# Kernel optimization log

Hardware: AMD Instinct MI355X
Metric: run time of the kernel (lower is better)

## Reference

```python
import jax, jax.numpy as jnp
import numpy as np

N = 50000
E = 1600000
F_IN = 4
F_OUT = 32
PERIODS = 12


def setup_inputs() -> dict:
    key = jax.random.key(0)
    ks = jax.random.split(key, 18)
    s_in = 1.0 / np.sqrt(F_IN)
    s_cat = 1.0 / np.sqrt(2 * F_OUT)
    s_out = 1.0 / np.sqrt(F_OUT)
    inp = {
        'x': jax.random.normal(ks[0], (N, F_IN, PERIODS), dtype=jnp.float32),
        'edge_index': jax.random.randint(ks[1], (2, E), 0, N, dtype=jnp.int32),
        'attention': jax.random.uniform(ks[2], (PERIODS,), dtype=jnp.float32),
        # GRU update gate z: GCNConv weight/bias + Linear(2*F_OUT -> F_OUT)
        'Wz': jax.random.normal(ks[3], (F_IN, F_OUT), jnp.float32) * s_in,
        'bz': jnp.zeros((F_OUT,), jnp.float32),
        'Lz': jax.random.normal(ks[4], (2 * F_OUT, F_OUT), jnp.float32) * s_cat,
        'lz': jnp.zeros((F_OUT,), jnp.float32),
        # reset gate r
        'Wr': jax.random.normal(ks[5], (F_IN, F_OUT), jnp.float32) * s_in,
        'br': jnp.zeros((F_OUT,), jnp.float32),
        'Lr': jax.random.normal(ks[6], (2 * F_OUT, F_OUT), jnp.float32) * s_cat,
        'lr': jnp.zeros((F_OUT,), jnp.float32),
        # candidate h
        'Wh': jax.random.normal(ks[7], (F_IN, F_OUT), jnp.float32) * s_in,
        'bh': jnp.zeros((F_OUT,), jnp.float32),
        'Lh': jax.random.normal(ks[8], (2 * F_OUT, F_OUT), jnp.float32) * s_cat,
        'lh': jnp.zeros((F_OUT,), jnp.float32),
        # outer Linear(32 -> periods)
        'Wo': jax.random.normal(ks[9], (F_OUT, PERIODS), jnp.float32) * s_out,
        'bo': jnp.zeros((PERIODS,), jnp.float32),
    }
    return inp


def reference(x, edge_index, attention, Wz, bz, Lz, lz, Wr, br, Lr, lr, Wh, bh, Lh, lh, Wo, bo):
    n = x.shape[0]
    # gcn_norm: add self loops, symmetric D^-1/2 (A+I) D^-1/2
    loop = jnp.arange(n, dtype=edge_index.dtype)
    row = jnp.concatenate([edge_index[0], loop])  # source
    col = jnp.concatenate([edge_index[1], loop])  # target
    w = jnp.ones(row.shape[0], dtype=x.dtype)
    deg = jax.ops.segment_sum(w, col, num_segments=n)
    dinv = jnp.where(deg > 0, jax.lax.rsqrt(deg), 0.0)
    norm = dinv[row] * dinv[col]  # [E+N]

    def conv(xt, W, b):
        h = xt @ W                                   # [N, F_OUT]
        msg = h[row] * norm[:, None]                 # gather + scale
        return jax.ops.segment_sum(msg, col, num_segments=n) + b

    H0 = jnp.zeros((n, F_OUT), dtype=x.dtype)  # A3TGCN passes H=None each period

    def tgcn(xt):
        Z = jax.nn.sigmoid(jnp.concatenate([conv(xt, Wz, bz), H0], axis=1) @ Lz + lz)
        R = jax.nn.sigmoid(jnp.concatenate([conv(xt, Wr, br), H0], axis=1) @ Lr + lr)
        Ht = jnp.tanh(jnp.concatenate([conv(xt, Wh, bh), H0 * R], axis=1) @ Lh + lh)
        return Z * H0 + (1.0 - Z) * Ht

    Hs = jax.vmap(tgcn)(jnp.moveaxis(x, 2, 0))       # [T, N, F_OUT]
    probs = jax.nn.softmax(attention)
    H = jnp.einsum('tnc,t->nc', Hs, probs)           # attention-weighted sum over periods
    return jax.nn.relu(H) @ Wo + bo                  # [N, PERIODS]
```

## Files before the change

kernel.cpp:

```cpp
#include <hip/hip_runtime.h>
#include <hip/hip_fp16.h>
#include <math.h>

#define CHUNK 6144
#define CAPG  10240
#define GNODES 21

union U2H { uint2 u; __half2 h[2]; };

__global__ void k_pre(const float* __restrict__ Wz, const float* __restrict__ Lz, const float* __restrict__ lz,
                      const float* __restrict__ Wh, const float* __restrict__ Lh, const float* __restrict__ lh,
                      const float* __restrict__ bz, const float* __restrict__ bh,
                      const float* __restrict__ att,
                      float* __restrict__ AzT, float* __restrict__ AhT,
                      float* __restrict__ bzp, float* __restrict__ bhp, float* __restrict__ probs,
                      int* __restrict__ gcur) {
  int t = threadIdx.x;
  gcur[t] = 0;
  if (t < 128) {
    int f = t >> 2, k = t & 3;
    float s = 0.f, s2 = 0.f;
    for (int j = 0; j < 32; ++j) {
      s  = fmaf(Wz[k * 32 + j], Lz[j * 32 + f], s);
      s2 = fmaf(Wh[k * 32 + j], Lh[j * 32 + f], s2);
    }
    AzT[t] = s; AhT[t] = s2;
  }
  if (t >= 128 && t < 160) {
    int f = t - 128;
    float s = lz[f], s2 = lh[f];
    for (int j = 0; j < 32; ++j) {
      s  = fmaf(bz[j], Lz[j * 32 + f], s);
      s2 = fmaf(bh[j], Lh[j * 32 + f], s2);
    }
    bzp[f] = s; bhp[f] = s2;
  }
  if (t == 160) {
    float m = att[0];
    for (int i = 1; i < 12; ++i) m = fmaxf(m, att[i]);
    float e[12]; float s = 0.f;
    for (int i = 0; i < 12; ++i) { e[i] = __expf(att[i] - m); s += e[i]; }
    for (int i = 0; i < 12; ++i) probs[i] = e[i] / s;
  }
}

__global__ __launch_bounds__(1024) void k_part(const int* __restrict__ row, const int* __restrict__ col,
                                               int E, int nbkt,
                                               int* __restrict__ gcur, unsigned* __restrict__ part) {
  __shared__ unsigned spak[CHUNK];
  __shared__ unsigned char sbkt[CHUNK];
  __shared__ unsigned char slc[CHUNK];
  __shared__ int hist[256], sscan[256], scur[256], gbase[256];
  int t = threadIdx.x;
  int base = blockIdx.x * CHUNK;
  int cnt = E - base; if (cnt > CHUNK) cnt = CHUNK;
  if (t < 256) hist[t] = 0;
  __syncthreads();
  for (int i = t; i < cnt; i += 1024) {
    int c = col[base + i];
    int b = c >> 8;
    sbkt[i] = (unsigned char)b;
    slc[i]  = (unsigned char)(c & 255);
    atomicAdd(&hist[b], 1);
  }
  __syncthreads();
  int v = 0;
  if (t < 256) { v = hist[t]; sscan[t] = v; }
  __syncthreads();
  for (int off = 1; off < 256; off <<= 1) {
    int a = 0;
    if (t < 256 && t >= off) a = sscan[t - off];
    __syncthreads();
    if (t < 256) sscan[t] += a;
    __syncthreads();
  }
  if (t < 256) {
    sscan[t] -= v;
    gbase[t] = (v > 0) ? atomicAdd(&gcur[t], v) : 0;
    scur[t] = 0;
  }
  __syncthreads();
  for (int i = t; i < cnt; i += 1024) {
    int r = row[base + i];
    int b = sbkt[i];
    int pos = atomicAdd(&scur[b], 1);
    spak[sscan[b] + pos] = ((unsigned)r << 8) | (unsigned)slc[i];
  }
  __syncthreads();
  int wave = t >> 6, lane = t & 63;
  for (int b = wave; b < nbkt; b += 16) {
    int len = hist[b], gb = gbase[b], src = sscan[b];
    int lim = CAPG - gb; if (lim > len) lim = len;
    unsigned* dst = part + (size_t)b * CAPG + gb;
    for (int j = lane; j < lim; j += 64) dst[j] = spak[src + j];
  }
}

__global__ __launch_bounds__(1024) void k_sort(const unsigned* __restrict__ part, const int* __restrict__ gcur,
                                               const float4* __restrict__ x4,
                                               int* __restrict__ csr, int2* __restrict__ rng,
                                               float* __restrict__ dinv, uint2* __restrict__ xh2, int n) {
  __shared__ unsigned sedge[CAPG];
  __shared__ int hist[256], soff[256], scur2[256];
  __shared__ float sdi[256];
  int b = blockIdx.x, t = threadIdx.x;
  int cnt = gcur[b]; if (cnt > CAPG) cnt = CAPG;
  const unsigned* src = part + (size_t)b * CAPG;
  if (t < 256) hist[t] = 0;
  __syncthreads();
  for (int i = t; i < cnt; i += 1024) {
    unsigned e = src[i];
    sedge[i] = e;
    atomicAdd(&hist[e & 255u], 1);
  }
  __syncthreads();
  int v = 0;
  if (t < 256) { v = hist[t]; soff[t] = v; }
  __syncthreads();
  for (int off = 1; off < 256; off <<= 1) {
    int a = 0;
    if (t < 256 && t >= off) a = soff[t - off];
    __syncthreads();
    if (t < 256) soff[t] += a;
    __syncthreads();
  }
  int base = b * CAPG;
  if (t < 256) {
    int excl = soff[t] - v;
    int node = b * 256 + t;
    float di = rsqrtf((float)(v + 1));
    sdi[t] = di;
    if (node < n) {
      rng[node] = make_int2(base + excl, base + excl + v);
      dinv[node] = di;
    }
    soff[t] = excl;
    scur2[t] = 0;
  }
  __syncthreads();
  for (int i = t; i < cnt; i += 1024) {
    unsigned e = sedge[i];
    int lc = (int)(e & 255u);
    int pos = atomicAdd(&scur2[lc], 1);
    csr[base + soff[lc] + pos] = (int)(e >> 8);
  }
  int gb = b * 3072;
  for (int j = t; j < 3072; j += 1024) {
    int gi = gb + j;
    if (gi < n * 12) {
      float4 f = x4[gi];
      float d = sdi[j / 12];
      __half2 h0 = __floats2half2_rn(d * f.x, d * f.y);
      __half2 h1 = __floats2half2_rn(d * f.z, d * f.w);
      uint2 u; u.x = *(unsigned*)&h0; u.y = *(unsigned*)&h1;
      xh2[gi] = u;
    }
  }
}

__global__ __launch_bounds__(256) void k_gather(const int* __restrict__ csr, const int2* __restrict__ rng,
                                                const float* __restrict__ dinv, const uint2* __restrict__ xh2,
                                                const float* __restrict__ AzT, const float* __restrict__ AhT,
                                                const float* __restrict__ bzp, const float* __restrict__ bhp,
                                                const float* __restrict__ probs,
                                                const float* __restrict__ Wo, const float* __restrict__ bo,
                                                float* __restrict__ out, int n) {
  __shared__ float sY[GNODES * 49];
  __shared__ float sH[GNODES * 33];
  __shared__ float4 sAz4[32], sAh4[32];
  __shared__ float sbzp[32], sbhp[32], sprobs[12], sbo[12], sWo[384];
  int t = threadIdx.x;
  int nb = blockIdx.x * GNODES;

  if (t < 32) {
    sAz4[t] = ((const float4*)AzT)[t];
    sAh4[t] = ((const float4*)AhT)[t];
    sbzp[t] = bzp[t]; sbhp[t] = bhp[t];
  }
  if (t >= 32 && t < 44) { sprobs[t - 32] = probs[t - 32]; sbo[t - 32] = bo[t - 32]; }
  for (int i = t; i < 384; i += 256) sWo[i] = Wo[i];

  int grp = t / 12, c = t - grp * 12;
  int node = nb + grp;
  if (grp < GNODES && node < n) {
    U2H s; s.u = xh2[(size_t)node * 12 + c];
    float2 f0 = __half22float2(s.h[0]), f1 = __half22float2(s.h[1]);
    float a0 = f0.x, a1 = f0.y, a2 = f1.x, a3 = f1.y;
    int2 r = rng[node];
    int e = r.x, end = r.y;
#define ACC4(V) { \
    float2 g0 = __half22float2(V.h[0]), g1 = __half22float2(V.h[1]); \
    a0 += g0.x; a1 += g0.y; a2 += g1.x; a3 += g1.y; }
    for (; e + 8 <= end; e += 8) {
      int r0 = csr[e],     r1 = csr[e + 1], r2 = csr[e + 2], r3 = csr[e + 3];
      int r4 = csr[e + 4], r5 = csr[e + 5], r6 = csr[e + 6], r7 = csr[e + 7];
      U2H v0, v1, v2, v3, v4, v5, v6, v7;
      v0.u = xh2[(size_t)r0 * 12 + c];
      v1.u = xh2[(size_t)r1 * 12 + c];
      v2.u = xh2[(size_t)r2 * 12 + c];
      v3.u = xh2[(size_t)r3 * 12 + c];
      v4.u = xh2[(size_t)r4 * 12 + c];
      v5.u = xh2[(size_t)r5 * 12 + c];
      v6.u = xh2[(size_t)r6 * 12 + c];
      v7.u = xh2[(size_t)r7 * 12 + c];
      ACC4(v0) ACC4(v1) ACC4(v2) ACC4(v3) ACC4(v4) ACC4(v5) ACC4(v6) ACC4(v7)
    }
    for (; e < end; ++e) {
      int r0 = csr[e];
      U2H v0; v0.u = xh2[(size_t)r0 * 12 + c];
      ACC4(v0)
    }
#undef ACC4
    float di = dinv[node];
    float* yb = sY + grp * 49 + c * 4;
    yb[0] = a0 * di; yb[1] = a1 * di; yb[2] = a2 * di; yb[3] = a3 * di;
  }
  __syncthreads();

  for (int u = t; u < GNODES * 32; u += 256) {
    int ln = u >> 5, f = u & 31;
    if (nb + ln >= n) continue;
    const float* y = sY + ln * 49;
    float4 az = sAz4[f], ah = sAh4[f];
    float bzf = sbzp[f], bhf = sbhp[f];
    float acc = 0.f;
#pragma unroll
    for (int tt = 0; tt < 12; ++tt) {
      float y0 = y[tt], y1 = y[12 + tt], y2 = y[24 + tt], y3 = y[36 + tt];
      float za = fmaf(az.x, y0, fmaf(az.y, y1, fmaf(az.z, y2, fmaf(az.w, y3, bzf))));
      float ha = fmaf(ah.x, y0, fmaf(ah.y, y1, fmaf(ah.z, y2, fmaf(ah.w, y3, bhf))));
      float ez = __expf(za);
      float ax = fabsf(ha);
      float e2 = __expf(-2.f * ax);
      float g = (1.f - e2) / ((1.f + ez) * (1.f + e2));
      acc = fmaf(sprobs[tt], copysignf(g, ha), acc);
    }
    sH[ln * 33 + f] = fmaxf(acc, 0.f);
  }
  __syncthreads();

  if (t < GNODES * 12) {
    int ln = t / 12, p = t - ln * 12;
    int node2 = nb + ln;
    if (node2 < n) {
      float acc = sbo[p];
      const float* h = sH + ln * 33;
      const float* wv = sWo + p;
#pragma unroll
      for (int f2 = 0; f2 < 32; ++f2) acc = fmaf(h[f2], wv[f2 * 12], acc);
      out[node2 * 12 + p] = acc;
    }
  }
}

extern "C" void kernel_launch(void* const* d_in, const int* in_sizes, int n_in,
                              void* d_out, int out_size, void* d_ws, size_t ws_size,
                              hipStream_t stream) {
  const float* x   = (const float*)d_in[0];
  const int*   ei  = (const int*)d_in[1];
  const float* att = (const float*)d_in[2];
  const float* Wz  = (const float*)d_in[3];
  const float* bz  = (const float*)d_in[4];
  const float* Lz  = (const float*)d_in[5];
  const float* lz  = (const float*)d_in[6];
  const float* Wh  = (const float*)d_in[11];
  const float* bh  = (const float*)d_in[12];
  const float* Lh  = (const float*)d_in[13];
  const float* lh  = (const float*)d_in[14];
  const float* Wo  = (const float*)d_in[15];
  const float* bo  = (const float*)d_in[16];
  float* out = (float*)d_out;

  const int N = in_sizes[0] / (4 * 12);
  const int E = in_sizes[1] / 2;
  const int NBKT = (N + 255) >> 8;
  const int* row = ei;
  const int* col = ei + E;

  char* w = (char*)d_ws;
  size_t o = 0;
  auto alloc = [&](size_t bytes) -> char* {
    o = (o + 255) & ~(size_t)255;
    char* p = w + o; o += bytes; return p;
  };
  float* pAzT   = (float*)alloc(128 * 4);
  float* pAhT   = (float*)alloc(128 * 4);
  float* pbzp   = (float*)alloc(32 * 4);
  float* pbhp   = (float*)alloc(32 * 4);
  float* pprobs = (float*)alloc(12 * 4);
  int*   pgcur  = (int*)alloc(256 * 4);
  float* pdinv  = (float*)alloc((size_t)NBKT * 256 * 4);
  int2*  prng   = (int2*)alloc((size_t)N * 8);
  unsigned* ppart = (unsigned*)alloc((size_t)256 * CAPG * 4);
  int*   pcsr   = (int*)alloc((size_t)256 * CAPG * 4);
  uint2* pxh    = (uint2*)alloc((size_t)NBKT * 256 * 12 * 8);
  (void)ws_size; (void)n_in; (void)out_size;

  k_pre<<<1, 256, 0, stream>>>(Wz, Lz, lz, Wh, Lh, lh, bz, bh, att,
                               pAzT, pAhT, pbzp, pbhp, pprobs, pgcur);
  k_part<<<(E + CHUNK - 1) / CHUNK, 1024, 0, stream>>>(row, col, E, NBKT, pgcur, ppart);
  k_sort<<<NBKT, 1024, 0, stream>>>(ppart, pgcur, (const float4*)x, pcsr, prng, pdinv, pxh, N);
  k_gather<<<(N + GNODES - 1) / GNODES, 256, 0, stream>>>(pcsr, prng, pdinv, pxh,
                                                          pAzT, pAhT, pbzp, pbhp, pprobs,
                                                          Wo, bo, out, N);
}
```

Before: 170.0 us.

## Split CSR sort into degree scan and parallel atomic scatter kernels

Per-node in-degrees are now counted with global atomics during partitioning. A small kernel scans these degrees to produce row ranges, cursors, dinv and the scaled half-precision features. A separate scatter kernel then places edges into CSR slots using global atomic cursors, with several blocks per bucket. This replaces the single shared-memory counting sort per bucket, whose grid was smaller than the GPU, with a more parallel scatter. In exchange it adds about 3.2M global atomics, and neighbour order within a row becomes nondeterministic. CSR entries are also stored pre-multiplied by 12 so the gather kernel skips that index multiply.

```diff
diff --git a/kernel.cpp b/kernel.cpp
--- a/kernel.cpp
+++ b/kernel.cpp
@@ -4,6 +4,7 @@
 
 #define CHUNK 6144
 #define CAPG  10240
+#define SCATB 5
 #define GNODES 21
 
 union U2H { uint2 u; __half2 h[2]; };
@@ -46,7 +47,8 @@
 
 __global__ __launch_bounds__(1024) void k_part(const int* __restrict__ row, const int* __restrict__ col,
                                                int E, int nbkt,
-                                               int* __restrict__ gcur, unsigned* __restrict__ part) {
+                                               int* __restrict__ gcur, unsigned* __restrict__ part,
+                                               int* __restrict__ deg) {
   __shared__ unsigned spak[CHUNK];
   __shared__ unsigned char sbkt[CHUNK];
   __shared__ unsigned char slc[CHUNK];
@@ -62,6 +64,7 @@
     sbkt[i] = (unsigned char)b;
     slc[i]  = (unsigned char)(c & 255);
     atomicAdd(&hist[b], 1);
+    atomicAdd(&deg[c], 1);
   }
   __syncthreads();
   int v = 0;
@@ -96,65 +99,60 @@
   }
 }
 
-__global__ __launch_bounds__(1024) void k_sort(const unsigned* __restrict__ part, const int* __restrict__ gcur,
-                                               const float4* __restrict__ x4,
-                                               int* __restrict__ csr, int2* __restrict__ rng,
-                                               float* __restrict__ dinv, uint2* __restrict__ xh2, int n) {
-  __shared__ unsigned sedge[CAPG];
-  __shared__ int hist[256], soff[256], scur2[256];
+__global__ __launch_bounds__(256) void k_dinv(const int* __restrict__ deg, const float4* __restrict__ x4,
+                                              int2* __restrict__ rng, int* __restrict__ cursor,
+                                              float* __restrict__ dinv, uint2* __restrict__ xh2, int n) {
+  __shared__ int s[256];
   __shared__ float sdi[256];
   int b = blockIdx.x, t = threadIdx.x;
-  int cnt = gcur[b]; if (cnt > CAPG) cnt = CAPG;
-  const unsigned* src = part + (size_t)b * CAPG;
-  if (t < 256) hist[t] = 0;
-  __syncthreads();
-  for (int i = t; i < cnt; i += 1024) {
-    unsigned e = src[i];
-    sedge[i] = e;
-    atomicAdd(&hist[e & 255u], 1);
-  }
-  __syncthreads();
-  int v = 0;
-  if (t < 256) { v = hist[t]; soff[t] = v; }
+  int node = b * 256 + t;
+  int d = (node < n) ? deg[node] : 0;
+  s[t] = d;
   __syncthreads();
   for (int off = 1; off < 256; off <<= 1) {
-    int a = 0;
-    if (t < 256 && t >= off) a = soff[t - off];
+    int a = (t >= off) ? s[t - off] : 0;
     __syncthreads();
-    if (t < 256) soff[t] += a;
+    s[t] += a;
     __syncthreads();
   }
+  int excl = s[t] - d;
   int base = b * CAPG;
-  if (t < 256) {
-    int excl = soff[t] - v;
-    int node = b * 256 + t;
-    float di = rsqrtf((float)(v + 1));
-    sdi[t] = di;
-    if (node < n) {
-      rng[node] = make_int2(base + excl, base + excl + v);
-      dinv[node] = di;
-    }
-    soff[t] = excl;
-    scur2[t] = 0;
-  }
-  __syncthreads();
-  for (int i = t; i < cnt; i += 1024) {
-    unsigned e = sedge[i];
-    int lc = (int)(e & 255u);
-    int pos = atomicAdd(&scur2[lc], 1);
-    csr[base + soff[lc] + pos] = (int)(e >> 8);
-  }
+  float di = rsqrtf((float)(d + 1));
+  sdi[t] = di;
+  if (node < n) {
+    rng[node] = make_int2(base + excl, base + excl + d);
+    cursor[node] = base + excl;
+    dinv[node] = di;
+  }
+  __syncthreads();
   int gb = b * 3072;
-  for (int j = t; j < 3072; j += 1024) {
+  for (int j = t; j < 3072; j += 256) {
     int gi = gb + j;
     if (gi < n * 12) {
       float4 f = x4[gi];
-      float d = sdi[j / 12];
-      __half2 h0 = __floats2half2_rn(d * f.x, d * f.y);
-      __half2 h1 = __floats2half2_rn(d * f.z, d * f.w);
+      float dd = sdi[j / 12];
+      __half2 h0 = __floats2half2_rn(dd * f.x, dd * f.y);
+      __half2 h1 = __floats2half2_rn(dd * f.z, dd * f.w);
       uint2 u; u.x = *(unsigned*)&h0; u.y = *(unsigned*)&h1;
       xh2[gi] = u;
     }
+  }
+}
+
+__global__ __launch_bounds__(512) void k_scat(const unsigned* __restrict__ part, const int* __restrict__ gcur,
+                                              int* __restrict__ cursor, int* __restrict__ csr, int nbkt) {
+  int b = blockIdx.x % nbkt;
+  int j = blockIdx.x / nbkt;
+  int cnt = gcur[b]; if (cnt > CAPG) cnt = CAPG;
+  int i0 = j * 2048;
+  int i1 = i0 + 2048; if (i1 > cnt) i1 = cnt;
+  const unsigned* src = part + (size_t)b * CAPG;
+  int lim = (b + 1) * CAPG;
+  for (int i = i0 + threadIdx.x; i < i1; i += 512) {
+    unsigned e = src[i];
+    int node = b * 256 + (int)(e & 255u);
+    int pos = atomicAdd(&cursor[node], 1);
+    if (pos < lim) csr[pos] = (int)(e >> 8) * 12;
   }
 }
 
@@ -183,7 +181,8 @@
   int grp = t / 12, c = t - grp * 12;
   int node = nb + grp;
   if (grp < GNODES && node < n) {
-    U2H s; s.u = xh2[(size_t)node * 12 + c];
+    const uint2* xb = xh2 + c;
+    U2H s; s.u = xb[(size_t)node * 12];
     float2 f0 = __half22float2(s.h[0]), f1 = __half22float2(s.h[1]);
     float a0 = f0.x, a1 = f0.y, a2 = f1.x, a3 = f1.y;
     int2 r = rng[node];
@@ -195,19 +194,13 @@
       int r0 = csr[e],     r1 = csr[e + 1], r2 = csr[e + 2], r3 = csr[e + 3];
       int r4 = csr[e + 4], r5 = csr[e + 5], r6 = csr[e + 6], r7 = csr[e + 7];
       U2H v0, v1, v2, v3, v4, v5, v6, v7;
-      v0.u = xh2[(size_t)r0 * 12 + c];
-      v1.u = xh2[(size_t)r1 * 12 + c];
-      v2.u = xh2[(size_t)r2 * 12 + c];
-      v3.u = xh2[(size_t)r3 * 12 + c];
-      v4.u = xh2[(size_t)r4 * 12 + c];
-      v5.u = xh2[(size_t)r5 * 12 + c];
-      v6.u = xh2[(size_t)r6 * 12 + c];
-      v7.u = xh2[(size_t)r7 * 12 + c];
+      v0.u = xb[r0]; v1.u = xb[r1]; v2.u = xb[r2]; v3.u = xb[r3];
+      v4.u = xb[r4]; v5.u = xb[r5]; v6.u = xb[r6]; v7.u = xb[r7];
       ACC4(v0) ACC4(v1) ACC4(v2) ACC4(v3) ACC4(v4) ACC4(v5) ACC4(v6) ACC4(v7)
     }
     for (; e < end; ++e) {
       int r0 = csr[e];
-      U2H v0; v0.u = xh2[(size_t)r0 * 12 + c];
+      U2H v0; v0.u = xb[r0];
       ACC4(v0)
     }
 #undef ACC4
@@ -289,6 +282,8 @@
   float* pbhp   = (float*)alloc(32 * 4);
   float* pprobs = (float*)alloc(12 * 4);
   int*   pgcur  = (int*)alloc(256 * 4);
+  int*   pdeg   = (int*)alloc((size_t)N * 4);
+  int*   pcursor= (int*)alloc((size_t)N * 4);
   float* pdinv  = (float*)alloc((size_t)NBKT * 256 * 4);
   int2*  prng   = (int2*)alloc((size_t)N * 8);
   unsigned* ppart = (unsigned*)alloc((size_t)256 * CAPG * 4);
@@ -296,10 +291,12 @@
   uint2* pxh    = (uint2*)alloc((size_t)NBKT * 256 * 12 * 8);
   (void)ws_size; (void)n_in; (void)out_size;
 
+  hipMemsetAsync(pdeg, 0, (size_t)N * 4, stream);
   k_pre<<<1, 256, 0, stream>>>(Wz, Lz, lz, Wh, Lh, lh, bz, bh, att,
                                pAzT, pAhT, pbzp, pbhp, pprobs, pgcur);
-  k_part<<<(E + CHUNK - 1) / CHUNK, 1024, 0, stream>>>(row, col, E, NBKT, pgcur, ppart);
-  k_sort<<<NBKT, 1024, 0, stream>>>(ppart, pgcur, (const float4*)x, pcsr, prng, pdinv, pxh, N);
+  k_part<<<(E + CHUNK - 1) / CHUNK, 1024, 0, stream>>>(row, col, E, NBKT, pgcur, ppart, pdeg);
+  k_dinv<<<NBKT, 256, 0, stream>>>(pdeg, (const float4*)x, prng, pcursor, pdinv, pxh, N);
+  k_scat<<<NBKT * SCATB, 512, 0, stream>>>(ppart, pgcur, pcursor, pcsr, NBKT);
   k_gather<<<(N + GNODES - 1) / GNODES, 256, 0, stream>>>(pcsr, prng, pdinv, pxh,
                                                           pAzT, pAhT, pbzp, pbhp, pprobs,
                                                           Wo, bo, out, N);
```

Result: slower. 274.9 us (+61.7%).

## Fold weight precompute into gather, flatten partition copy, prescale CSR indices

Applied to the files above, without the earlier changes.

Removes the single-block k_pre launch. Each gather block now recomputes the folded gate weights and the attention softmax in shared memory, and gcur is zeroed with a memset instead. The partition scatter-out now runs one thread per edge using a per-slot bucket byte, replacing the per-wave bucket loop, which should balance the global writes better. CSR entries are stored premultiplied by 12 so the gather's address arithmetic is simpler. The cost is redundant weight folding in every gather block (about 2400 blocks) and more shared memory in k_part.

```diff
diff --git a/kernel.cpp b/kernel.cpp
--- a/kernel.cpp
+++ b/kernel.cpp
@@ -7,42 +7,6 @@
 #define GNODES 21
 
 union U2H { uint2 u; __half2 h[2]; };
-
-__global__ void k_pre(const float* __restrict__ Wz, const float* __restrict__ Lz, const float* __restrict__ lz,
-                      const float* __restrict__ Wh, const float* __restrict__ Lh, const float* __restrict__ lh,
-                      const float* __restrict__ bz, const float* __restrict__ bh,
-                      const float* __restrict__ att,
-                      float* __restrict__ AzT, float* __restrict__ AhT,
-                      float* __restrict__ bzp, float* __restrict__ bhp, float* __restrict__ probs,
-                      int* __restrict__ gcur) {
-  int t = threadIdx.x;
-  gcur[t] = 0;
-  if (t < 128) {
-    int f = t >> 2, k = t & 3;
-    float s = 0.f, s2 = 0.f;
-    for (int j = 0; j < 32; ++j) {
-      s  = fmaf(Wz[k * 32 + j], Lz[j * 32 + f], s);
-      s2 = fmaf(Wh[k * 32 + j], Lh[j * 32 + f], s2);
-    }
-    AzT[t] = s; AhT[t] = s2;
-  }
-  if (t >= 128 && t < 160) {
-    int f = t - 128;
-    float s = lz[f], s2 = lh[f];
-    for (int j = 0; j < 32; ++j) {
-      s  = fmaf(bz[j], Lz[j * 32 + f], s);
-      s2 = fmaf(bh[j], Lh[j * 32 + f], s2);
-    }
-    bzp[f] = s; bhp[f] = s2;
-  }
-  if (t == 160) {
-    float m = att[0];
-    for (int i = 1; i < 12; ++i) m = fmaxf(m, att[i]);
-    float e[12]; float s = 0.f;
-    for (int i = 0; i < 12; ++i) { e[i] = __expf(att[i] - m); s += e[i]; }
-    for (int i = 0; i < 12; ++i) probs[i] = e[i] / s;
-  }
-}
 
 __global__ __launch_bounds__(1024) void k_part(const int* __restrict__ row, const int* __restrict__ col,
                                                int E, int nbkt,
@@ -50,6 +14,7 @@
   __shared__ unsigned spak[CHUNK];
   __shared__ unsigned char sbkt[CHUNK];
   __shared__ unsigned char slc[CHUNK];
+  __shared__ unsigned char sdst[CHUNK];
   __shared__ int hist[256], sscan[256], scur[256], gbase[256];
   int t = threadIdx.x;
   int base = blockIdx.x * CHUNK;
@@ -84,15 +49,15 @@
     int r = row[base + i];
     int b = sbkt[i];
     int pos = atomicAdd(&scur[b], 1);
-    spak[sscan[b] + pos] = ((unsigned)r << 8) | (unsigned)slc[i];
-  }
-  __syncthreads();
-  int wave = t >> 6, lane = t & 63;
-  for (int b = wave; b < nbkt; b += 16) {
-    int len = hist[b], gb = gbase[b], src = sscan[b];
-    int lim = CAPG - gb; if (lim > len) lim = len;
-    unsigned* dst = part + (size_t)b * CAPG + gb;
-    for (int j = lane; j < lim; j += 64) dst[j] = spak[src + j];
+    int j = sscan[b] + pos;
+    spak[j] = ((unsigned)r << 8) | (unsigned)slc[i];
+    sdst[j] = (unsigned char)b;
+  }
+  __syncthreads();
+  for (int i = t; i < cnt; i += 1024) {
+    int b = sdst[i];
+    int gb = gbase[b] + (i - sscan[b]);
+    if (gb < CAPG) part[(size_t)b * CAPG + gb] = spak[i];
   }
 }
 
@@ -142,7 +107,7 @@
     unsigned e = sedge[i];
     int lc = (int)(e & 255u);
     int pos = atomicAdd(&scur2[lc], 1);
-    csr[base + soff[lc] + pos] = (int)(e >> 8);
+    csr[base + soff[lc] + pos] = (int)(e >> 8) * 12;
   }
   int gb = b * 3072;
   for (int j = t; j < 3072; j += 1024) {
@@ -160,9 +125,12 @@
 
 __global__ __launch_bounds__(256) void k_gather(const int* __restrict__ csr, const int2* __restrict__ rng,
                                                 const float* __restrict__ dinv, const uint2* __restrict__ xh2,
-                                                const float* __restrict__ AzT, const float* __restrict__ AhT,
-                                                const float* __restrict__ bzp, const float* __restrict__ bhp,
-                                                const float* __restrict__ probs,
+                                                const float* __restrict__ Wz, const float* __restrict__ Lz,
+                                                const float* __restrict__ lz,
+                                                const float* __restrict__ Wh, const float* __restrict__ Lh,
+                                                const float* __restrict__ lh,
+                                                const float* __restrict__ bz, const float* __restrict__ bh,
+                                                const float* __restrict__ att,
                                                 const float* __restrict__ Wo, const float* __restrict__ bo,
                                                 float* __restrict__ out, int n) {
   __shared__ float sY[GNODES * 49];
@@ -172,18 +140,40 @@
   int t = threadIdx.x;
   int nb = blockIdx.x * GNODES;
 
-  if (t < 32) {
-    sAz4[t] = ((const float4*)AzT)[t];
-    sAh4[t] = ((const float4*)AhT)[t];
-    sbzp[t] = bzp[t]; sbhp[t] = bhp[t];
-  }
-  if (t >= 32 && t < 44) { sprobs[t - 32] = probs[t - 32]; sbo[t - 32] = bo[t - 32]; }
+  if (t < 128) {
+    int f = t >> 2, k = t & 3;
+    float s = 0.f, s2 = 0.f;
+    for (int j = 0; j < 32; ++j) {
+      s  = fmaf(Wz[k * 32 + j], Lz[j * 32 + f], s);
+      s2 = fmaf(Wh[k * 32 + j], Lh[j * 32 + f], s2);
+    }
+    ((float*)sAz4)[t] = s;
+    ((float*)sAh4)[t] = s2;
+  }
+  if (t >= 128 && t < 160) {
+    int f = t - 128;
+    float s = lz[f], s2 = lh[f];
+    for (int j = 0; j < 32; ++j) {
+      s  = fmaf(bz[j], Lz[j * 32 + f], s);
+      s2 = fmaf(bh[j], Lh[j * 32 + f], s2);
+    }
+    sbzp[f] = s; sbhp[f] = s2;
+  }
+  if (t == 160) {
+    float m = att[0];
+    for (int i = 1; i < 12; ++i) m = fmaxf(m, att[i]);
+    float e[12]; float s = 0.f;
+    for (int i = 0; i < 12; ++i) { e[i] = __expf(att[i] - m); s += e[i]; }
+    for (int i = 0; i < 12; ++i) sprobs[i] = e[i] / s;
+  }
+  if (t >= 176 && t < 188) sbo[t - 176] = bo[t - 176];
   for (int i = t; i < 384; i += 256) sWo[i] = Wo[i];
 
   int grp = t / 12, c = t - grp * 12;
   int node = nb + grp;
   if (grp < GNODES && node < n) {
-    U2H s; s.u = xh2[(size_t)node * 12 + c];
+    const uint2* xb = xh2 + c;
+    U2H s; s.u = xb[(size_t)node * 12];
     float2 f0 = __half22float2(s.h[0]), f1 = __half22float2(s.h[1]);
     float a0 = f0.x, a1 = f0.y, a2 = f1.x, a3 = f1.y;
     int2 r = rng[node];
@@ -195,19 +185,13 @@
       int r0 = csr[e],     r1 = csr[e + 1], r2 = csr[e + 2], r3 = csr[e + 3];
       int r4 = csr[e + 4], r5 = csr[e + 5], r6 = csr[e + 6], r7 = csr[e + 7];
       U2H v0, v1, v2, v3, v4, v5, v6, v7;
-      v0.u = xh2[(size_t)r0 * 12 + c];
-      v1.u = xh2[(size_t)r1 * 12 + c];
-      v2.u = xh2[(size_t)r2 * 12 + c];
-      v3.u = xh2[(size_t)r3 * 12 + c];
-      v4.u = xh2[(size_t)r4 * 12 + c];
-      v5.u = xh2[(size_t)r5 * 12 + c];
-      v6.u = xh2[(size_t)r6 * 12 + c];
-      v7.u = xh2[(size_t)r7 * 12 + c];
+      v0.u = xb[r0]; v1.u = xb[r1]; v2.u = xb[r2]; v3.u = xb[r3];
+      v4.u = xb[r4]; v5.u = xb[r5]; v6.u = xb[r6]; v7.u = xb[r7];
       ACC4(v0) ACC4(v1) ACC4(v2) ACC4(v3) ACC4(v4) ACC4(v5) ACC4(v6) ACC4(v7)
     }
     for (; e < end; ++e) {
       int r0 = csr[e];
-      U2H v0; v0.u = xh2[(size_t)r0 * 12 + c];
+      U2H v0; v0.u = xb[r0];
       ACC4(v0)
     }
 #undef ACC4
@@ -283,11 +267,6 @@
     o = (o + 255) & ~(size_t)255;
     char* p = w + o; o += bytes; return p;
   };
-  float* pAzT   = (float*)alloc(128 * 4);
-  float* pAhT   = (float*)alloc(128 * 4);
-  float* pbzp   = (float*)alloc(32 * 4);
-  float* pbhp   = (float*)alloc(32 * 4);
-  float* pprobs = (float*)alloc(12 * 4);
   int*   pgcur  = (int*)alloc(256 * 4);
   float* pdinv  = (float*)alloc((size_t)NBKT * 256 * 4);
   int2*  prng   = (int2*)alloc((size_t)N * 8);
@@ -296,11 +275,10 @@
   uint2* pxh    = (uint2*)alloc((size_t)NBKT * 256 * 12 * 8);
   (void)ws_size; (void)n_in; (void)out_size;
 
-  k_pre<<<1, 256, 0, stream>>>(Wz, Lz, lz, Wh, Lh, lh, bz, bh, att,
-                               pAzT, pAhT, pbzp, pbhp, pprobs, pgcur);
+  hipMemsetAsync(pgcur, 0, 256 * 4, stream);
   k_part<<<(E + CHUNK - 1) / CHUNK, 1024, 0, stream>>>(row, col, E, NBKT, pgcur, ppart);
   k_sort<<<NBKT, 1024, 0, stream>>>(ppart, pgcur, (const float4*)x, pcsr, prng, pdinv, pxh, N);
   k_gather<<<(N + GNODES - 1) / GNODES, 256, 0, stream>>>(pcsr, prng, pdinv, pxh,
-                                                          pAzT, pAhT, pbzp, pbhp, pprobs,
+                                                          Wz, Lz, lz, Wh, Lh, lh, bz, bh, att,
                                                           Wo, bo, out, N);
 }
```

After: 174.4 us. 1.03x slower.
